# Optimization experiments

Measured on AMD Instinct MI355X. Metric: run time of the kernel, lower is better.

Reference implementation:

```python
import jax, jax.numpy as jnp
import numpy as np

N = 50000   # nodes
E = 800000  # edges
F = 128     # feat_dim
LN_EPS = 1e-5


def setup_inputs() -> dict:
    key = jax.random.key(0)
    ks = jax.random.split(key, 16)

    def lin(k, fan_in, shape):
        # roughly kaiming-uniform-like scale; exact init is irrelevant for correctness
        return jax.random.normal(k, shape, jnp.float32) * (1.0 / np.sqrt(fan_in))

    inp = {
        "x": jax.random.normal(ks[0], (N, F), jnp.float32),
        "pos": jax.random.normal(ks[1], (N, 3), jnp.float32),
        "edge_index": jax.random.randint(ks[2], (2, E), 0, N, jnp.int64),
        # edge_mlp: Linear(2F+1 -> F), SiLU, Linear(F -> F)
        "ew1": lin(ks[3], 2 * F + 1, (2 * F + 1, F)),
        "eb1": jnp.zeros((F,), jnp.float32),
        "ew2": lin(ks[4], F, (F, F)),
        "eb2": jnp.zeros((F,), jnp.float32),
        # node_mlp: Linear(F -> F), SiLU, Linear(F -> F)
        "nw1": lin(ks[5], F, (F, F)),
        "nb1": jnp.zeros((F,), jnp.float32),
        "nw2": lin(ks[6], F, (F, F)),
        "nb2": jnp.zeros((F,), jnp.float32),
        # coord_mlp: Linear(F -> 1), Tanh
        "cw": lin(ks[7], F, (F, 1)),
        "cb": jnp.zeros((1,), jnp.float32),
        # LayerNorm(F)
        "gamma": jnp.ones((F,), jnp.float32),
        "beta": jnp.zeros((F,), jnp.float32),
    }
    return inp


def reference(x, pos, edge_index, ew1, eb1, ew2, eb2, nw1, nb1, nw2, nb2, cw, cb, gamma, beta):
    row, col = edge_index[0], edge_index[1]

    diff = pos[row] - pos[col]                              # [E, 3]
    dist2 = jnp.sum(diff * diff, axis=1, keepdims=True)     # [E, 1]
    edge_feat = jnp.concatenate([x[row], x[col], dist2], axis=1)  # [E, 2F+1]

    # edge MLP (dropout p=0 -> identity in eval)
    msg = jax.nn.silu(edge_feat @ ew1 + eb1) @ ew2 + eb2    # [E, F]

    # scatter-add messages to source nodes
    agg = jax.ops.segment_sum(msg, row, num_segments=N)     # [N, F]

    # node MLP + residual + LayerNorm
    upd = jax.nn.silu(agg @ nw1 + nb1) @ nw2 + nb2          # [N, F]
    pre = x + upd
    mean = jnp.mean(pre, axis=-1, keepdims=True)
    var = jnp.mean(jnp.square(pre - mean), axis=-1, keepdims=True)
    x_out = gamma * (pre - mean) * jax.lax.rsqrt(var + LN_EPS) + beta

    # coordinate update
    scale = jnp.tanh(msg @ cw + cb)                         # [E, 1]
    delta = jax.ops.segment_sum(scale * diff, row, num_segments=N)  # [N, 3]
    pos_out = pos + delta
    return (x_out, pos_out)
```

## Files before the change

kernel.cpp:

```cpp
#include <hip/hip_runtime.h>
#include <math.h>

#define NN 50000
#define EE 800000
#define FF 128

constexpr float LN_EPS = 1e-5f;
constexpr int NC = (NN + 255) / 256;

typedef float  f32x4  __attribute__((ext_vector_type(4)));
typedef short  s16x8  __attribute__((ext_vector_type(8)));

__device__ __forceinline__ float silu_f(float v) {
    return v / (1.f + __expf(-v));
}

__device__ __forceinline__ unsigned short f2bf(float f) {
    union { float f; unsigned u; } cv; cv.f = f;
    unsigned u = cv.u;
    u += 0x7fffu + ((u >> 16) & 1u);
    return (unsigned short)(u >> 16);
}

__device__ __forceinline__ float bf2f(unsigned short u) {
    union { unsigned u; float f; } cv; cv.u = ((unsigned)u) << 16;
    return cv.f;
}

__global__ __launch_bounds__(256) void convert_x_kernel(
    const float* __restrict__ x, unsigned short* __restrict__ xb)
{
    int i = (blockIdx.x * 256 + threadIdx.x) * 8;
    float4 a = *(const float4*)&x[i];
    float4 b = *(const float4*)&x[i + 4];
    s16x8 o;
    o[0] = (short)f2bf(a.x); o[1] = (short)f2bf(a.y);
    o[2] = (short)f2bf(a.z); o[3] = (short)f2bf(a.w);
    o[4] = (short)f2bf(b.x); o[5] = (short)f2bf(b.y);
    o[6] = (short)f2bf(b.z); o[7] = (short)f2bf(b.w);
    *(s16x8*)&xb[i] = o;
}

__global__ __launch_bounds__(256) void transpose_w_kernel(
    const float* __restrict__ ew1, const float* __restrict__ ew2,
    const float* __restrict__ nw1, const float* __restrict__ nw2,
    unsigned short* __restrict__ ew1T, unsigned short* __restrict__ ew2T,
    unsigned short* __restrict__ nw1T, unsigned short* __restrict__ nw2T)
{
    int o = blockIdx.x * 256 + threadIdx.x;
    if (o < 32768) {
        int n = o >> 8, k = o & 255;
        ew1T[o] = f2bf(ew1[k * FF + n]);
    } else if (o < 49152) {
        int o2 = o - 32768; int n = o2 >> 7, k = o2 & 127;
        ew2T[o2] = f2bf(ew2[k * FF + n]);
    } else if (o < 65536) {
        int o2 = o - 49152; int n = o2 >> 7, k = o2 & 127;
        nw1T[o2] = f2bf(nw1[k * FF + n]);
    } else {
        int o2 = o - 65536; int n = o2 >> 7, k = o2 & 127;
        nw2T[o2] = f2bf(nw2[k * FF + n]);
    }
}

__global__ __launch_bounds__(256) void hist_kernel(
    const int* __restrict__ ei, int* __restrict__ cnt)
{
    int e = blockIdx.x * 256 + threadIdx.x;
    if (e < EE) atomicAdd(&cnt[ei[e]], 1);
}

__global__ __launch_bounds__(256) void chunk_sum_kernel(
    const int* __restrict__ cnt, int* __restrict__ chunkSum)
{
    __shared__ int s[256];
    int t = threadIdx.x;
    int idx = blockIdx.x * 256 + t;
    s[t] = (idx < NN) ? cnt[idx] : 0;
    __syncthreads();
    for (int off = 128; off > 0; off >>= 1) {
        if (t < off) s[t] += s[t + off];
        __syncthreads();
    }
    if (t == 0) chunkSum[blockIdx.x] = s[0];
}

__global__ __launch_bounds__(256) void scan_chunks_kernel(
    const int* __restrict__ chunkSum, int* __restrict__ chunkOff)
{
    __shared__ int s[256];
    int t = threadIdx.x;
    int v = (t < NC) ? chunkSum[t] : 0;
    s[t] = v;
    __syncthreads();
    for (int off = 1; off < 256; off <<= 1) {
        int u = (t >= off) ? s[t - off] : 0;
        __syncthreads();
        s[t] += u;
        __syncthreads();
    }
    if (t < NC) chunkOff[t] = s[t] - v;
}

__global__ __launch_bounds__(256) void scan_kernel(
    const int* __restrict__ cnt, const int* __restrict__ chunkOff,
    int* __restrict__ offs, int* __restrict__ rowStart)
{
    __shared__ int s[256];
    int t = threadIdx.x;
    int idx = blockIdx.x * 256 + t;
    int v = (idx < NN) ? cnt[idx] : 0;
    s[t] = v;
    __syncthreads();
    for (int off = 1; off < 256; off <<= 1) {
        int u = (t >= off) ? s[t - off] : 0;
        __syncthreads();
        s[t] += u;
        __syncthreads();
    }
    if (idx < NN) {
        int st = chunkOff[blockIdx.x] + s[t] - v;
        offs[idx] = st;
        rowStart[idx] = st;
    }
}

__global__ __launch_bounds__(256) void scatter_idx_kernel(
    const int* __restrict__ ei, int* __restrict__ offs,
    int* __restrict__ sRow, int* __restrict__ sCol)
{
    int e = blockIdx.x * 256 + threadIdx.x;
    if (e < EE) {
        int r = ei[e], c = ei[EE + e];
        int p = atomicAdd(&offs[r], 1);
        sRow[p] = r;
        sCol[p] = c;
    }
}

constexpr int EPB   = 64;
constexpr int NTILE = EE / EPB;
constexpr int XAS   = 264;
constexpr int H1S   = 136;

__global__ __launch_bounds__(512, 4) void edgeA_kernel(
    const unsigned short* __restrict__ xb, const float* __restrict__ pos,
    const int* __restrict__ sRow, const int* __restrict__ sCol,
    const unsigned short* __restrict__ ew1T, const float* __restrict__ ew1,
    const float* __restrict__ eb1,
    const unsigned short* __restrict__ ew2T, const float* __restrict__ eb2,
    const float* __restrict__ cw,  const float* __restrict__ cb,
    unsigned short* __restrict__ msgb, float* __restrict__ sSg)
{
    __shared__ float dist2S[EPB];
    __shared__ float sPart[8][EPB];
    __shared__ __align__(16) unsigned short xa  [EPB * XAS];
    __shared__ __align__(16) unsigned short h1  [EPB * H1S];
    __shared__ __align__(16) unsigned short msgL[EPB * H1S];

    const int t   = threadIdx.x;
    const int w   = t >> 6;
    const int l   = t & 63;
    const int l15 = l & 15;
    const int q8  = l >> 4;
    const int n   = w * 16 + l15;

    s16x8 B1[8], B2[4];
    #pragma unroll
    for (int ko = 0; ko < 8; ++ko)
        B1[ko] = *(const s16x8*)(ew1T + (size_t)n * 256 + ko * 32 + q8 * 8);
    #pragma unroll
    for (int ko = 0; ko < 4; ++ko)
        B2[ko] = *(const s16x8*)(ew2T + (size_t)n * 128 + ko * 32 + q8 * 8);
    const float w256 = ew1[256 * FF + n];
    const float b1   = eb1[n];
    const float b2   = eb2[n];
    const float cwc  = cw[n];
    const float cb0  = cb[0];

    const int q   = t & 31;
    const int eB  = t >> 5;
    const int ksel = (q & 15) * 8;
    const int* idxBase = (q < 16) ? sRow : sCol;

    int   nidx[4];
    s16x8 ag[4];
    {
        int e0 = blockIdx.x * EPB;
        #pragma unroll
        for (int i = 0; i < 4; ++i) nidx[i] = idxBase[e0 + eB + 16 * i];
        #pragma unroll
        for (int i = 0; i < 4; ++i) ag[i] = *(const s16x8*)(xb + (size_t)nidx[i] * FF + ksel);
    }

    for (int tile = blockIdx.x; tile < NTILE; tile += gridDim.x) {
        const int e0 = tile * EPB;

        #pragma unroll
        for (int i = 0; i < 4; ++i)
            *(s16x8*)(xa + (eB + 16 * i) * XAS + q * 8) = ag[i];
        if (t < EPB) {
            int r = sRow[e0 + t];
            int c = sCol[e0 + t];
            float dx = pos[r*3+0] - pos[c*3+0];
            float dy = pos[r*3+1] - pos[c*3+1];
            float dz = pos[r*3+2] - pos[c*3+2];
            dist2S[t] = dx*dx + dy*dy + dz*dz;
        }
        __syncthreads();

        {
            int tn  = tile + gridDim.x;
            int e0n = (tn < NTILE) ? tn * EPB : 0;
            #pragma unroll
            for (int i = 0; i < 4; ++i) nidx[i] = idxBase[e0n + eB + 16 * i];
            #pragma unroll
            for (int i = 0; i < 4; ++i) ag[i] = *(const s16x8*)(xb + (size_t)nidx[i] * FF + ksel);
        }

        f32x4 acc[4] = {};
        #pragma unroll
        for (int mt = 0; mt < 4; ++mt) {
            const unsigned short* ar = xa + (mt * 16 + l15) * XAS + q8 * 8;
            #pragma unroll
            for (int ko = 0; ko < 8; ++ko) {
                s16x8 a = *(const s16x8*)(ar + ko * 32);
                acc[mt] = __builtin_amdgcn_mfma_f32_16x16x32_bf16(a, B1[ko], acc[mt], 0, 0, 0);
            }
        }

        #pragma unroll
        for (int mt = 0; mt < 4; ++mt) {
            #pragma unroll
            for (int r = 0; r < 4; ++r) {
                int e = mt * 16 + q8 * 4 + r;
                float v = acc[mt][r] + dist2S[e] * w256 + b1;
                h1[e * H1S + n] = f2bf(silu_f(v));
            }
        }
        __syncthreads();

        f32x4 acc2[4] = {};
        #pragma unroll
        for (int mt = 0; mt < 4; ++mt) {
            const unsigned short* hr = h1 + (mt * 16 + l15) * H1S + q8 * 8;
            #pragma unroll
            for (int ko = 0; ko < 4; ++ko) {
                s16x8 a = *(const s16x8*)(hr + ko * 32);
                acc2[mt] = __builtin_amdgcn_mfma_f32_16x16x32_bf16(a, B2[ko], acc2[mt], 0, 0, 0);
            }
        }

        #pragma unroll
        for (int mt = 0; mt < 4; ++mt) {
            #pragma unroll
            for (int r = 0; r < 4; ++r) {
                float m = acc2[mt][r] + b2;
                float p = m * cwc;
                p += __shfl_xor(p, 1);
                p += __shfl_xor(p, 2);
                p += __shfl_xor(p, 4);
                p += __shfl_xor(p, 8);
                int e = mt * 16 + q8 * 4 + r;
                if (l15 == 0) sPart[w][e] = p;
                msgL[e * H1S + n] = f2bf(m);
            }
        }
        __syncthreads();

        if (t < EPB) {
            float p = 0.f;
            #pragma unroll
            for (int ww = 0; ww < 8; ++ww) p += sPart[ww][t];
            sSg[e0 + t] = tanhf(p + cb0);
        }

        #pragma unroll
        for (int i = 0; i < 2; ++i) {
            int idx = i * 512 + t;
            int e   = idx >> 4;
            int c   = idx & 15;
            *(s16x8*)&msgb[(size_t)(e0 + e) * FF + c * 8] =
                *(const s16x8*)&msgL[e * H1S + c * 8];
        }
    }
}

constexpr int NPB = 16;
constexpr int ABS = 136;

__global__ __launch_bounds__(512) void nodeB_kernel(
    const float* __restrict__ x, const float* __restrict__ pos,
    const unsigned short* __restrict__ msgb, const float* __restrict__ sSg,
    const int* __restrict__ sCol, const int* __restrict__ rowStart,
    const unsigned short* __restrict__ nw1T, const float* __restrict__ nb1,
    const unsigned short* __restrict__ nw2T, const float* __restrict__ nb2,
    const float* __restrict__ gamma, const float* __restrict__ beta,
    float* __restrict__ xout, float* __restrict__ posout)
{
    __shared__ __align__(16) unsigned short aB [NPB * ABS];
    __shared__ __align__(16) unsigned short h1B[NPB * ABS];
    __shared__ float sRedS[8][NPB];
    __shared__ float sRedQ[8][NPB];

    const int t   = threadIdx.x;
    const int w   = t >> 6;
    const int l   = t & 63;
    const int l15 = l & 15;
    const int q8  = l >> 4;
    const int n0  = blockIdx.x * NPB;
    const int n   = w * 16 + l15;

    #pragma unroll
    for (int s = 0; s < 2; ++s) {
        int e  = 2 * w + s;
        int nn = n0 + e;
        int p0 = rowStart[nn];
        int p1 = (nn == NN - 1) ? EE : rowStart[nn + 1];
        float a0=0.f,a1=0.f,a2=0.f,a3=0.f,a4=0.f,a5=0.f,a6=0.f,a7=0.f;
        for (int p = p0 + q8; p < p1; p += 4) {
            s16x8 v = *(const s16x8*)(msgb + (size_t)p * FF + l15 * 8);
            a0 += bf2f((unsigned short)v[0]);
            a1 += bf2f((unsigned short)v[1]);
            a2 += bf2f((unsigned short)v[2]);
            a3 += bf2f((unsigned short)v[3]);
            a4 += bf2f((unsigned short)v[4]);
            a5 += bf2f((unsigned short)v[5]);
            a6 += bf2f((unsigned short)v[6]);
            a7 += bf2f((unsigned short)v[7]);
        }
        a0 += __shfl_xor(a0,16); a1 += __shfl_xor(a1,16);
        a2 += __shfl_xor(a2,16); a3 += __shfl_xor(a3,16);
        a4 += __shfl_xor(a4,16); a5 += __shfl_xor(a5,16);
        a6 += __shfl_xor(a6,16); a7 += __shfl_xor(a7,16);
        a0 += __shfl_xor(a0,32); a1 += __shfl_xor(a1,32);
        a2 += __shfl_xor(a2,32); a3 += __shfl_xor(a3,32);
        a4 += __shfl_xor(a4,32); a5 += __shfl_xor(a5,32);
        a6 += __shfl_xor(a6,32); a7 += __shfl_xor(a7,32);
        if (q8 == 0) {
            s16x8 o;
            o[0]=(short)f2bf(a0); o[1]=(short)f2bf(a1);
            o[2]=(short)f2bf(a2); o[3]=(short)f2bf(a3);
            o[4]=(short)f2bf(a4); o[5]=(short)f2bf(a5);
            o[6]=(short)f2bf(a6); o[7]=(short)f2bf(a7);
            *(s16x8*)(aB + e * ABS + l15 * 8) = o;
        }
    }

    if (t < NPB * 3) {
        int e = t / 3, d = t % 3;
        int nn = n0 + e;
        int p0 = rowStart[nn];
        int p1 = (nn == NN - 1) ? EE : rowStart[nn + 1];
        float pn = pos[nn * 3 + d];
        float sum = 0.f;
        for (int p = p0; p < p1; ++p) {
            int c = sCol[p];
            sum += sSg[p] * (pn - pos[c * 3 + d]);
        }
        posout[nn * 3 + d] = pn + sum;
    }
    __syncthreads();

    f32x4 acc = {};
    {
        const unsigned short* ar = aB + l15 * ABS + q8 * 8;
        #pragma unroll
        for (int ko = 0; ko < 4; ++ko) {
            s16x8 a = *(const s16x8*)(ar + ko * 32);
            s16x8 b = *(const s16x8*)(nw1T + (size_t)n * 128 + ko * 32 + q8 * 8);
            acc = __builtin_amdgcn_mfma_f32_16x16x32_bf16(a, b, acc, 0, 0, 0);
        }
    }
    {
        float bb = nb1[n];
        #pragma unroll
        for (int r = 0; r < 4; ++r) {
            int e = q8 * 4 + r;
            h1B[e * ABS + n] = f2bf(silu_f(acc[r] + bb));
        }
    }
    __syncthreads();

    f32x4 acc2 = {};
    {
        const unsigned short* hr = h1B + l15 * ABS + q8 * 8;
        #pragma unroll
        for (int ko = 0; ko < 4; ++ko) {
            s16x8 a = *(const s16x8*)(hr + ko * 32);
            s16x8 b = *(const s16x8*)(nw2T + (size_t)n * 128 + ko * 32 + q8 * 8);
            acc2 = __builtin_amdgcn_mfma_f32_16x16x32_bf16(a, b, acc2, 0, 0, 0);
        }
    }

    float pre[4];
    {
        float bb = nb2[n];
        #pragma unroll
        for (int r = 0; r < 4; ++r) {
            int e = q8 * 4 + r;
            pre[r] = x[(size_t)(n0 + e) * FF + n] + acc2[r] + bb;
        }
    }
    #pragma unroll
    for (int r = 0; r < 4; ++r) {
        float s = pre[r], sq = pre[r] * pre[r];
        s += __shfl_xor(s, 1);  sq += __shfl_xor(sq, 1);
        s += __shfl_xor(s, 2);  sq += __shfl_xor(sq, 2);
        s += __shfl_xor(s, 4);  sq += __shfl_xor(sq, 4);
        s += __shfl_xor(s, 8);  sq += __shfl_xor(sq, 8);
        if (l15 == 0) {
            int e = q8 * 4 + r;
            sRedS[w][e] = s;
            sRedQ[w][e] = sq;
        }
    }
    __syncthreads();

    {
        float g = gamma[n], bt = beta[n];
        #pragma unroll
        for (int r = 0; r < 4; ++r) {
            int e = q8 * 4 + r;
            float S = 0.f, Q = 0.f;
            #pragma unroll
            for (int ww = 0; ww < 8; ++ww) { S += sRedS[ww][e]; Q += sRedQ[ww][e]; }
            float mean = S * (1.f / FF);
            float var  = Q * (1.f / FF) - mean * mean;
            xout[(size_t)(n0 + e) * FF + n] =
                g * (pre[r] - mean) * rsqrtf(var + LN_EPS) + bt;
        }
    }
}

extern "C" void kernel_launch(void* const* d_in, const int* in_sizes, int n_in,
                              void* d_out, int out_size, void* d_ws, size_t ws_size,
                              hipStream_t stream) {
    const float* x    = (const float*)d_in[0];
    const float* pos  = (const float*)d_in[1];
    const int*   ei   = (const int*)  d_in[2];
    const float* ew1  = (const float*)d_in[3];
    const float* eb1  = (const float*)d_in[4];
    const float* ew2  = (const float*)d_in[5];
    const float* eb2  = (const float*)d_in[6];
    const float* nw1  = (const float*)d_in[7];
    const float* nb1  = (const float*)d_in[8];
    const float* nw2  = (const float*)d_in[9];
    const float* nb2  = (const float*)d_in[10];
    const float* cw   = (const float*)d_in[11];
    const float* cb   = (const float*)d_in[12];
    const float* gam  = (const float*)d_in[13];
    const float* bet  = (const float*)d_in[14];

    float* out    = (float*)d_out;
    float* xout   = out;
    float* posout = out + (size_t)NN * FF;

    auto align256 = [](size_t v) { return (v + 255) & ~(size_t)255; };
    char* ws = (char*)d_ws;

    size_t CNT_B   = align256((size_t)NN * 4);
    size_t OFFS_B  = align256((size_t)NN * 4);
    size_t RST_B   = align256((size_t)NN * 4);
    size_t CHNK_B  = align256((size_t)NC * 4 * 2);
    size_t SROW_B  = align256((size_t)EE * 4);
    size_t XB_B    = align256((size_t)NN * FF * 2);
    size_t EW1T_B  = align256((size_t)128 * 256 * 2);
    size_t WT_B    = align256((size_t)128 * 128 * 2);
    size_t MSGB_B  = align256((size_t)EE * FF * 2);

    size_t o = 0;
    int* cnt       = (int*)(ws + o);  o += CNT_B;
    int* offs      = (int*)(ws + o);  o += OFFS_B;
    int* rowStart  = (int*)(ws + o);  o += RST_B;
    int* chunkSum  = (int*)(ws + o);
    int* chunkOff  = chunkSum + NC;   o += CHNK_B;
    int* sRow      = (int*)(ws + o);  o += SROW_B;
    int* sCol      = (int*)(ws + o);  o += SROW_B;
    unsigned short* xb   = (unsigned short*)(ws + o);  o += XB_B;
    unsigned short* ew1T = (unsigned short*)(ws + o);  o += EW1T_B;
    unsigned short* ew2T = (unsigned short*)(ws + o);  o += WT_B;
    unsigned short* nw1T = (unsigned short*)(ws + o);  o += WT_B;
    unsigned short* nw2T = (unsigned short*)(ws + o);  o += WT_B;
    unsigned short* msgb = (unsigned short*)(ws + o);  o += MSGB_B;
    float*          sSg  = (float*)(ws + o);

    hipMemsetAsync(cnt, 0, CNT_B, stream);

    convert_x_kernel<<<(NN * FF / 8) / 256, 256, 0, stream>>>(x, xb);
    transpose_w_kernel<<<(32768 + 3 * 16384) / 256, 256, 0, stream>>>(
        ew1, ew2, nw1, nw2, ew1T, ew2T, nw1T, nw2T);

    hist_kernel<<<(EE + 255) / 256, 256, 0, stream>>>(ei, cnt);
    chunk_sum_kernel<<<NC, 256, 0, stream>>>(cnt, chunkSum);
    scan_chunks_kernel<<<1, 256, 0, stream>>>(chunkSum, chunkOff);
    scan_kernel<<<NC, 256, 0, stream>>>(cnt, chunkOff, offs, rowStart);
    scatter_idx_kernel<<<(EE + 255) / 256, 256, 0, stream>>>(ei, offs, sRow, sCol);

    edgeA_kernel<<<2048, 512, 0, stream>>>(
        xb, pos, sRow, sCol, ew1T, ew1, eb1, ew2T, eb2, cw, cb, msgb, sSg);

    nodeB_kernel<<<NN / NPB, 512, 0, stream>>>(
        x, pos, msgb, sSg, sCol, rowStart,
        nw1T, nb1, nw2T, nb2, gam, bet, xout, posout);
}
```

Before: 536.7 us.

## Fuse message segment-sum into edge kernel via sorted-run atomics

The edge kernel no longer writes per-edge bf16 messages to global memory. Because edges are sorted by row, it sums runs of equal row inside each tile and does float atomicAdds into an fp32 node aggregate buffer, which is zeroed up front. The node kernel then reads that aggregate directly instead of reducing message rows, and splits the position-delta loop across 4 lanes per dimension. This removes the ~200MB message write and its read-back, in exchange for global atomics, an extra memset and an extra barrier per tile.

```diff
diff --git a/kernel.cpp b/kernel.cpp
--- a/kernel.cpp
+++ b/kernel.cpp
@@ -10,6 +10,7 @@
 
 typedef float  f32x4  __attribute__((ext_vector_type(4)));
 typedef short  s16x8  __attribute__((ext_vector_type(8)));
+typedef unsigned short u16x4 __attribute__((ext_vector_type(4)));
 
 __device__ __forceinline__ float silu_f(float v) {
     return v / (1.f + __expf(-v));
@@ -150,9 +151,10 @@
     const float* __restrict__ eb1,
     const unsigned short* __restrict__ ew2T, const float* __restrict__ eb2,
     const float* __restrict__ cw,  const float* __restrict__ cb,
-    unsigned short* __restrict__ msgb, float* __restrict__ sSg)
+    float* __restrict__ agg, float* __restrict__ sSg)
 {
     __shared__ float dist2S[EPB];
+    __shared__ int   rowS  [EPB];
     __shared__ float sPart[8][EPB];
     __shared__ __align__(16) unsigned short xa  [EPB * XAS];
     __shared__ __align__(16) unsigned short h1  [EPB * H1S];
@@ -202,6 +204,7 @@
         if (t < EPB) {
             int r = sRow[e0 + t];
             int c = sCol[e0 + t];
+            rowS[t] = r;
             float dx = pos[r*3+0] - pos[c*3+0];
             float dy = pos[r*3+1] - pos[c*3+1];
             float dz = pos[r*3+2] - pos[c*3+2];
@@ -275,14 +278,25 @@
             sSg[e0 + t] = tanhf(p + cb0);
         }
 
-        #pragma unroll
-        for (int i = 0; i < 2; ++i) {
-            int idx = i * 512 + t;
-            int e   = idx >> 4;
-            int c   = idx & 15;
-            *(s16x8*)&msgb[(size_t)(e0 + e) * FF + c * 8] =
-                *(const s16x8*)&msgL[e * H1S + c * 8];
-        }
+        {
+            int c    = t & 127;
+            int s    = t >> 7;
+            int base = s * 16;
+            float a  = 0.f;
+            int cur  = rowS[base];
+            #pragma unroll
+            for (int k = 0; k < 16; ++k) {
+                int e = base + k;
+                int r = rowS[e];
+                if (r != cur) {
+                    atomicAdd(&agg[(size_t)cur * FF + c], a);
+                    a = 0.f; cur = r;
+                }
+                a += bf2f(msgL[e * H1S + c]);
+            }
+            atomicAdd(&agg[(size_t)cur * FF + c], a);
+        }
+        __syncthreads();
     }
 }
 
@@ -291,7 +305,7 @@
 
 __global__ __launch_bounds__(512) void nodeB_kernel(
     const float* __restrict__ x, const float* __restrict__ pos,
-    const unsigned short* __restrict__ msgb, const float* __restrict__ sSg,
+    const float* __restrict__ agg, const float* __restrict__ sSg,
     const int* __restrict__ sCol, const int* __restrict__ rowStart,
     const unsigned short* __restrict__ nw1T, const float* __restrict__ nb1,
     const unsigned short* __restrict__ nw2T, const float* __restrict__ nb2,
@@ -302,6 +316,7 @@
     __shared__ __align__(16) unsigned short h1B[NPB * ABS];
     __shared__ float sRedS[8][NPB];
     __shared__ float sRedQ[8][NPB];
+    __shared__ float sPosP[NPB][3][4];
 
     const int t   = threadIdx.x;
     const int w   = t >> 6;
@@ -311,56 +326,39 @@
     const int n0  = blockIdx.x * NPB;
     const int n   = w * 16 + l15;
 
-    #pragma unroll
-    for (int s = 0; s < 2; ++s) {
-        int e  = 2 * w + s;
-        int nn = n0 + e;
-        int p0 = rowStart[nn];
-        int p1 = (nn == NN - 1) ? EE : rowStart[nn + 1];
-        float a0=0.f,a1=0.f,a2=0.f,a3=0.f,a4=0.f,a5=0.f,a6=0.f,a7=0.f;
-        for (int p = p0 + q8; p < p1; p += 4) {
-            s16x8 v = *(const s16x8*)(msgb + (size_t)p * FF + l15 * 8);
-            a0 += bf2f((unsigned short)v[0]);
-            a1 += bf2f((unsigned short)v[1]);
-            a2 += bf2f((unsigned short)v[2]);
-            a3 += bf2f((unsigned short)v[3]);
-            a4 += bf2f((unsigned short)v[4]);
-            a5 += bf2f((unsigned short)v[5]);
-            a6 += bf2f((unsigned short)v[6]);
-            a7 += bf2f((unsigned short)v[7]);
-        }
-        a0 += __shfl_xor(a0,16); a1 += __shfl_xor(a1,16);
-        a2 += __shfl_xor(a2,16); a3 += __shfl_xor(a3,16);
-        a4 += __shfl_xor(a4,16); a5 += __shfl_xor(a5,16);
-        a6 += __shfl_xor(a6,16); a7 += __shfl_xor(a7,16);
-        a0 += __shfl_xor(a0,32); a1 += __shfl_xor(a1,32);
-        a2 += __shfl_xor(a2,32); a3 += __shfl_xor(a3,32);
-        a4 += __shfl_xor(a4,32); a5 += __shfl_xor(a5,32);
-        a6 += __shfl_xor(a6,32); a7 += __shfl_xor(a7,32);
-        if (q8 == 0) {
-            s16x8 o;
-            o[0]=(short)f2bf(a0); o[1]=(short)f2bf(a1);
-            o[2]=(short)f2bf(a2); o[3]=(short)f2bf(a3);
-            o[4]=(short)f2bf(a4); o[5]=(short)f2bf(a5);
-            o[6]=(short)f2bf(a6); o[7]=(short)f2bf(a7);
-            *(s16x8*)(aB + e * ABS + l15 * 8) = o;
-        }
-    }
+    {
+        int idx = t * 4;
+        int e = idx >> 7, c = idx & 127;
+        float4 v = *(const float4*)&agg[(size_t)(n0 + e) * FF + c];
+        u16x4 o;
+        o[0] = f2bf(v.x); o[1] = f2bf(v.y); o[2] = f2bf(v.z); o[3] = f2bf(v.w);
+        *(u16x4*)(aB + e * ABS + c) = o;
+    }
+
+    if (t < NPB * 12) {
+        int e   = t / 12;
+        int rem = t - e * 12;
+        int d   = rem % 3;
+        int ch  = rem / 3;
+        int nn  = n0 + e;
+        int p0  = rowStart[nn];
+        int p1  = (nn == NN - 1) ? EE : rowStart[nn + 1];
+        float pn = pos[nn * 3 + d];
+        float sum = 0.f;
+        for (int p = p0 + ch; p < p1; p += 4) {
+            int c = sCol[p];
+            sum += sSg[p] * (pn - pos[c * 3 + d]);
+        }
+        sPosP[e][d][ch] = sum;
+    }
+    __syncthreads();
 
     if (t < NPB * 3) {
         int e = t / 3, d = t % 3;
         int nn = n0 + e;
-        int p0 = rowStart[nn];
-        int p1 = (nn == NN - 1) ? EE : rowStart[nn + 1];
-        float pn = pos[nn * 3 + d];
-        float sum = 0.f;
-        for (int p = p0; p < p1; ++p) {
-            int c = sCol[p];
-            sum += sSg[p] * (pn - pos[c * 3 + d]);
-        }
-        posout[nn * 3 + d] = pn + sum;
-    }
-    __syncthreads();
+        posout[nn * 3 + d] = pos[nn * 3 + d]
+            + sPosP[e][d][0] + sPosP[e][d][1] + sPosP[e][d][2] + sPosP[e][d][3];
+    }
 
     f32x4 acc = {};
     {
@@ -467,7 +465,7 @@
     size_t XB_B    = align256((size_t)NN * FF * 2);
     size_t EW1T_B  = align256((size_t)128 * 256 * 2);
     size_t WT_B    = align256((size_t)128 * 128 * 2);
-    size_t MSGB_B  = align256((size_t)EE * FF * 2);
+    size_t AGG_B   = align256((size_t)NN * FF * 4);
 
     size_t o = 0;
     int* cnt       = (int*)(ws + o);  o += CNT_B;
@@ -482,10 +480,11 @@
     unsigned short* ew2T = (unsigned short*)(ws + o);  o += WT_B;
     unsigned short* nw1T = (unsigned short*)(ws + o);  o += WT_B;
     unsigned short* nw2T = (unsigned short*)(ws + o);  o += WT_B;
-    unsigned short* msgb = (unsigned short*)(ws + o);  o += MSGB_B;
+    float*          agg  = (float*)(ws + o);           o += AGG_B;
     float*          sSg  = (float*)(ws + o);
 
     hipMemsetAsync(cnt, 0, CNT_B, stream);
+    hipMemsetAsync(agg, 0, (size_t)NN * FF * 4, stream);
 
     convert_x_kernel<<<(NN * FF / 8) / 256, 256, 0, stream>>>(x, xb);
     transpose_w_kernel<<<(32768 + 3 * 16384) / 256, 256, 0, stream>>>(
@@ -498,9 +497,9 @@
     scatter_idx_kernel<<<(EE + 255) / 256, 256, 0, stream>>>(ei, offs, sRow, sCol);
 
     edgeA_kernel<<<2048, 512, 0, stream>>>(
-        xb, pos, sRow, sCol, ew1T, ew1, eb1, ew2T, eb2, cw, cb, msgb, sSg);
+        xb, pos, sRow, sCol, ew1T, ew1, eb1, ew2T, eb2, cw, cb, agg, sSg);
 
     nodeB_kernel<<<NN / NPB, 512, 0, stream>>>(
-        x, pos, msgb, sSg, sCol, rowStart,
+        x, pos, agg, sSg, sCol, rowStart,
         nw1T, nb1, nw2T, nb2, gam, bet, xout, posout);
 }
```

New measurement: 503.1 us. 6.3% less time.
